# Kernel optimization log

Measured on AMD Instinct MI355X. Metric: run time of the kernel, lower is better.

Reference implementation:

```python
import jax, jax.numpy as jnp
import numpy as np
from jax import lax

B, L, DM = 2, 1024, 1024
DIN, DSTATE, DCONV, DTRANK = 2048, 16, 4, 64


def setup_inputs() -> dict:
    key = jax.random.key(0)
    ks = jax.random.split(key, 8)
    s = 0.02
    x = jax.random.normal(ks[0], (B, L, DM), jnp.float32)
    in_proj_w = jax.random.normal(ks[1], (2 * DIN, DM), jnp.float32) * s
    conv_w = jax.random.normal(ks[2], (DIN, 1, DCONV), jnp.float32) * 0.2
    conv_b = jnp.zeros((DIN,), jnp.float32)
    x_proj_w = jax.random.normal(ks[3], (DTRANK + 2 * DSTATE, DIN), jnp.float32) * s
    dt_proj_w = jax.random.normal(ks[4], (DIN, DTRANK), jnp.float32) * s
    dt_proj_b = jnp.full((DIN,), -4.0, jnp.float32)  # small init dt after softplus
    # S4D-real init: A_log = log(1..d_state) per channel
    A_log = jnp.log(jnp.broadcast_to(jnp.arange(1, DSTATE + 1, dtype=jnp.float32), (DIN, DSTATE)))
    D_skip = jnp.ones((DIN,), jnp.float32)
    out_proj_w = jax.random.normal(ks[5], (DM, DIN), jnp.float32) * s
    return {
        "x": x, "norm_w": jnp.ones((DM,), jnp.float32), "norm_b": jnp.zeros((DM,), jnp.float32),
        "in_proj_w": in_proj_w, "conv_w": conv_w, "conv_b": conv_b,
        "x_proj_w": x_proj_w, "dt_proj_w": dt_proj_w, "dt_proj_b": dt_proj_b,
        "A_log": A_log, "D_skip": D_skip, "out_proj_w": out_proj_w,
    }


def _layernorm(x, w, b, eps=1e-5):
    mu = jnp.mean(x, axis=-1, keepdims=True)
    var = jnp.mean(jnp.square(x - mu), axis=-1, keepdims=True)
    return (x - mu) * lax.rsqrt(var + eps) * w + b


def _mamba(h, in_proj_w, conv_w, conv_b, x_proj_w, dt_proj_w, dt_proj_b, A_log, D_skip, out_proj_w):
    # h: [B, L, DM]
    xz = jnp.einsum('bld,ed->ble', h, in_proj_w)          # [B, L, 2*DIN]
    xm, z = jnp.split(xz, 2, axis=-1)                     # each [B, L, DIN]
    # causal depthwise conv1d over time
    xc = jnp.transpose(xm, (0, 2, 1))                     # [B, DIN, L]
    xc = jnp.pad(xc, ((0, 0), (0, 0), (DCONV - 1, 0)))
    xc = lax.conv_general_dilated(xc, conv_w, (1,), 'VALID',
                                  dimension_numbers=('NCH', 'OIH', 'NCH'),
                                  feature_group_count=DIN)
    xc = xc + conv_b[None, :, None]
    xc = jnp.transpose(xc, (0, 2, 1))                     # [B, L, DIN]
    xc = jax.nn.silu(xc)
    # input-dependent SSM parameters
    x_dbl = jnp.einsum('bld,ed->ble', xc, x_proj_w)       # [B, L, DTRANK+2N]
    dt, Bm, Cm = jnp.split(x_dbl, [DTRANK, DTRANK + DSTATE], axis=-1)
    dt = jax.nn.softplus(jnp.einsum('blr,dr->bld', dt, dt_proj_w) + dt_proj_b)  # [B, L, DIN]
    A = -jnp.exp(A_log)                                   # [DIN, N]
    deltaA = jnp.exp(dt[..., None] * A)                   # [B, L, DIN, N]
    deltaBu = dt[..., None] * Bm[:, :, None, :] * xc[..., None]  # [B, L, DIN, N]
    # sequential selective scan over time
    dA_t = jnp.transpose(deltaA, (1, 0, 2, 3))            # [L, B, DIN, N]
    dBu_t = jnp.transpose(deltaBu, (1, 0, 2, 3))
    C_t = jnp.transpose(Cm, (1, 0, 2))                    # [L, B, N]

    def step(hs, inp):
        dA, dBu, Ct = inp
        hs = dA * hs + dBu                                # [B, DIN, N]
        y = jnp.einsum('bdn,bn->bd', hs, Ct)
        return hs, y

    h0 = jnp.zeros((B, DIN, DSTATE), xc.dtype)
    _, ys = lax.scan(step, h0, (dA_t, dBu_t, C_t))        # ys: [L, B, DIN]
    y = jnp.transpose(ys, (1, 0, 2)) + xc * D_skip        # [B, L, DIN]
    y = y * jax.nn.silu(z)
    return jnp.einsum('bld,ed->ble', y, out_proj_w)       # [B, L, DM]


def reference(x, norm_w, norm_b, in_proj_w, conv_w, conv_b, x_proj_w,
              dt_proj_w, dt_proj_b, A_log, D_skip, out_proj_w):
    h = _layernorm(x, norm_w, norm_b)
    return x + _mamba(h, in_proj_w, conv_w, conv_b, x_proj_w,
                      dt_proj_w, dt_proj_b, A_log, D_skip, out_proj_w)
```

## Files before the change

### kernel.cpp

```cpp
#include <hip/hip_runtime.h>


typedef unsigned short u16;
typedef unsigned int u32;

typedef __bf16 bf16x8 __attribute__((ext_vector_type(8)));
typedef float f32x4 __attribute__((ext_vector_type(4)));

#define SCAN_G 8
#define NSTATE 65536

#if __has_builtin(__builtin_amdgcn_exp2f)
#define EXP2F(x) __builtin_amdgcn_exp2f(x)
#else
#define EXP2F(x) exp2f(x)
#endif
#define LOG2E 1.44269504f

__device__ __forceinline__ u16 f2bf(float f) {
  u32 u = __float_as_uint(f);
  u32 r = u + 0x7FFFu + ((u >> 16) & 1u);
  return (u16)(r >> 16);
}
__device__ __forceinline__ float bf2f(u16 v) {
  return __uint_as_float(((u32)v) << 16);
}

__device__ __forceinline__ void lds_load16(const u16* g, u16* l) {
  __builtin_amdgcn_global_load_lds(
      (const __attribute__((address_space(1))) u32*)g,
      (__attribute__((address_space(3))) u32*)l, 16, 0, 0);
}

__global__ __launch_bounds__(256) void convert_all_kernel(
    const float* __restrict__ w0, const float* __restrict__ w1,
    const float* __restrict__ w2, const float* __restrict__ w3,
    u16* __restrict__ o0, u16* __restrict__ o1,
    u16* __restrict__ o2, u16* __restrict__ o3) {
  const int i = blockIdx.x * 256 + threadIdx.x;
  if (i < 4194304) {
    o0[i] = f2bf(w0[i]);
  } else if (i < 4390912) {
    const int j = i - 4194304;
    o1[j] = f2bf(w1[j]);
  } else if (i < 4521984) {
    const int j = i - 4390912;
    o2[j] = f2bf(w2[j]);
  } else if (i < 6619136) {
    const int j = i - 4521984;
    o3[j] = f2bf(w3[j]);
  }
}

__global__ __launch_bounds__(256) void ln_bf16_kernel(
    const float* __restrict__ x, const float* __restrict__ w,
    const float* __restrict__ b, u16* __restrict__ h) {
  const int row = blockIdx.x;
  const int tid = threadIdx.x;
  const float4 v = ((const float4*)(x + (size_t)row * 1024))[tid];
  float s = v.x + v.y + v.z + v.w;
  float s2 = v.x * v.x + v.y * v.y + v.z * v.z + v.w * v.w;
  for (int off = 32; off >= 1; off >>= 1) {
    s += __shfl_xor(s, off);
    s2 += __shfl_xor(s2, off);
  }
  __shared__ float red[8];
  const int wave = tid >> 6;
  if ((tid & 63) == 0) { red[wave * 2] = s; red[wave * 2 + 1] = s2; }
  __syncthreads();
  s = red[0] + red[2] + red[4] + red[6];
  s2 = red[1] + red[3] + red[5] + red[7];
  const float mu = s * (1.0f / 1024.0f);
  const float var = s2 * (1.0f / 1024.0f) - mu * mu;
  const float rstd = rsqrtf(var + 1e-5f);
  const float4 wv = ((const float4*)w)[tid];
  const float4 bv = ((const float4*)b)[tid];
  ushort4 o;
  o.x = f2bf((v.x - mu) * rstd * wv.x + bv.x);
  o.y = f2bf((v.y - mu) * rstd * wv.y + bv.y);
  o.z = f2bf((v.z - mu) * rstd * wv.z + bv.z);
  o.w = f2bf((v.w - mu) * rstd * wv.w + bv.w);
  ((ushort4*)(h + (size_t)row * 1024))[tid] = o;
}

template <int EPI, int SPLITK>
__global__ __launch_bounds__(256) void gemm_bt(
    const u16* __restrict__ A, const u16* __restrict__ W,
    void* __restrict__ C, const float* __restrict__ extra,
    int M, int N, int K) {
  const int n0 = blockIdx.x * 64;
  const int m0 = blockIdx.y * 64;
  const int ks = (SPLITK > 1) ? blockIdx.z : 0;
  const int kLen = K / SPLITK;
  const int kOff = ks * kLen;
  __shared__ u16 As[64 * 32];
  __shared__ u16 Ws[64 * 32];
  const int tid = threadIdx.x;
  const int wave = tid >> 6;
  const int lane = tid & 63;
  const int wm = (wave >> 1) * 32;
  const int wn = (wave & 1) * 32;
  const int lrow = tid >> 2;
  const int lcg = (tid & 3) * 8;
  const int arow = m0 + lrow;
  const int wrow = n0 + lrow;
  f32x4 acc[2][2];
#pragma unroll
  for (int i = 0; i < 2; ++i)
#pragma unroll
    for (int j = 0; j < 2; ++j) acc[i][j] = (f32x4){0.f, 0.f, 0.f, 0.f};

  const int fm = lane & 15;
  const int fk = (lane >> 4) * 8;

  for (int k0 = kOff; k0 < kOff + kLen; k0 += 32) {
    uint4 av = *(const uint4*)(A + (size_t)arow * K + k0 + lcg);
    uint4 wv = make_uint4(0u, 0u, 0u, 0u);
    if (wrow < N) wv = *(const uint4*)(W + (size_t)wrow * K + k0 + lcg);
    __syncthreads();
    *(uint4*)(As + lrow * 32 + lcg) = av;
    *(uint4*)(Ws + lrow * 32 + lcg) = wv;
    __syncthreads();
    bf16x8 a0 = *(const bf16x8*)(As + (wm + fm) * 32 + fk);
    bf16x8 a1 = *(const bf16x8*)(As + (wm + 16 + fm) * 32 + fk);
    bf16x8 b0 = *(const bf16x8*)(Ws + (wn + fm) * 32 + fk);
    bf16x8 b1 = *(const bf16x8*)(Ws + (wn + 16 + fm) * 32 + fk);
    acc[0][0] = __builtin_amdgcn_mfma_f32_16x16x32_bf16(a0, b0, acc[0][0], 0, 0, 0);
    acc[0][1] = __builtin_amdgcn_mfma_f32_16x16x32_bf16(a0, b1, acc[0][1], 0, 0, 0);
    acc[1][0] = __builtin_amdgcn_mfma_f32_16x16x32_bf16(a1, b0, acc[1][0], 0, 0, 0);
    acc[1][1] = __builtin_amdgcn_mfma_f32_16x16x32_bf16(a1, b1, acc[1][1], 0, 0, 0);
  }

  const int col = lane & 15;
  const int rbase = (lane >> 4) * 4;
#pragma unroll
  for (int tm = 0; tm < 2; ++tm)
#pragma unroll
    for (int tn = 0; tn < 2; ++tn)
#pragma unroll
      for (int r = 0; r < 4; ++r) {
        int m = m0 + wm + tm * 16 + rbase + r;
        int n = n0 + wn + tn * 16 + col;
        if (n < N) {
          float v = acc[tm][tn][r];
          if (EPI == 0) {
            ((float*)C)[(size_t)ks * M * N + (size_t)m * N + n] = v;
          } else {
            v += extra[n];
            v = (v > 20.f) ? v : log1pf(__expf(v));
            ((u16*)C)[(size_t)m * N + n] = f2bf(v);
          }
        }
      }
}

template <int EPI, int SPLITK>
__global__ __launch_bounds__(256) void gemm128_kernel(
    const u16* __restrict__ A, const u16* __restrict__ W,
    u16* __restrict__ Cout, int M, int N, int K) {
  const int n0 = blockIdx.x * 128;
  const int m0 = blockIdx.y * 128;
  const int ks = (SPLITK > 1) ? blockIdx.z : 0;
  const int kLen = K / SPLITK;
  const int k0 = ks * kLen;
  __shared__ u16 As[128 * 32];
  __shared__ u16 Ws[128 * 32];
  const int tid = threadIdx.x;
  const int wave = tid >> 6;
  const int lane = tid & 63;
  const int wm = (wave >> 1) * 64;
  const int wn = (wave & 1) * 64;
  f32x4 acc[4][4];
#pragma unroll
  for (int i = 0; i < 4; ++i)
#pragma unroll
    for (int j = 0; j < 4; ++j) acc[i][j] = (f32x4){0.f, 0.f, 0.f, 0.f};

  const int fm = lane & 15;
  const int fk = (lane >> 4) * 8;
  const int sr = lane >> 2;
  const int sc = (lane & 3) * 8;
  const u16* gA = A + (size_t)(m0 + wave * 32 + sr) * K + k0 + sc;
  const u16* gB = W + (size_t)(n0 + wave * 32 + sr) * K + k0 + sc;
  u16* lA = As + wave * 1024;
  u16* lB = Ws + wave * 1024;

  for (int kk = 0; kk < kLen; kk += 32) {
    __syncthreads();
    lds_load16(gA + kk, lA);
    lds_load16(gA + (size_t)16 * K + kk, lA + 512);
    lds_load16(gB + kk, lB);
    lds_load16(gB + (size_t)16 * K + kk, lB + 512);
    __syncthreads();
    bf16x8 af[4], bfr[4];
#pragma unroll
    for (int i = 0; i < 4; ++i)
      af[i] = *(const bf16x8*)(As + (wm + i * 16 + fm) * 32 + fk);
#pragma unroll
    for (int j = 0; j < 4; ++j)
      bfr[j] = *(const bf16x8*)(Ws + (wn + j * 16 + fm) * 32 + fk);
#pragma unroll
    for (int i = 0; i < 4; ++i)
#pragma unroll
      for (int j = 0; j < 4; ++j)
        acc[i][j] = __builtin_amdgcn_mfma_f32_16x16x32_bf16(af[i], bfr[j], acc[i][j], 0, 0, 0);
  }

  const int col = lane & 15;
  const int rb = (lane >> 4) * 4;
#pragma unroll
  for (int i = 0; i < 4; ++i)
#pragma unroll
    for (int j = 0; j < 4; ++j)
#pragma unroll
      for (int r = 0; r < 4; ++r) {
        const int m = m0 + wm + i * 16 + rb + r;
        const int n = n0 + wn + j * 16 + col;
        if (EPI == 4)
          Cout[(size_t)m * N + n] = f2bf(acc[i][j][r]);
        else
          Cout[(size_t)ks * M * N + (size_t)m * N + n] = f2bf(acc[i][j][r]);
      }
}

__global__ __launch_bounds__(256) void xproj_comb_kernel(
    const float* __restrict__ part, float* __restrict__ xdbl,
    u16* __restrict__ dtr) {
  const int i = blockIdx.x * 256 + threadIdx.x;
  const float v = part[i] + part[i + 196608] + part[i + 2 * 196608] +
                  part[i + 3 * 196608];
  xdbl[i] = v;
  const int m = i / 96;
  const int c = i - m * 96;
  if (c < 64) dtr[(size_t)m * 64 + c] = f2bf(v);
}

__global__ __launch_bounds__(256) void out_comb_kernel(
    const u16* __restrict__ part, const float* __restrict__ x,
    float* __restrict__ out) {
  const int i4 = (blockIdx.x * 256 + threadIdx.x) * 4;
  const float4 xv = *(const float4*)&x[i4];
  float a0 = xv.x, a1 = xv.y, a2 = xv.z, a3 = xv.w;
#pragma unroll
  for (int ks = 0; ks < 4; ++ks) {
    ushort4 pv = *(const ushort4*)&part[(size_t)ks * 2097152 + i4];
    a0 += bf2f(pv.x); a1 += bf2f(pv.y); a2 += bf2f(pv.z); a3 += bf2f(pv.w);
  }
  float4 o = {a0, a1, a2, a3};
  *(float4*)&out[i4] = o;
}

__global__ __launch_bounds__(256) void conv_silu_kernel(
    const u16* __restrict__ xzb, const float* __restrict__ cw,
    const float* __restrict__ cb, u16* __restrict__ xcb) {
  const int idx = blockIdx.x * 256 + threadIdx.x;
  const int d = idx & 2047;
  const int m = idx >> 11;
  const int l = m & 1023;
  const float4 wv = ((const float4*)cw)[d];
  const float w4[4] = {wv.x, wv.y, wv.z, wv.w};
  float acc = cb[d];
#pragma unroll
  for (int k = 0; k < 4; ++k) {
    int lk = l + k - 3;
    if (lk >= 0) acc += bf2f(xzb[(size_t)(m + k - 3) * 4096 + d]) * w4[k];
  }
  const float sv = acc / (1.0f + __expf(-acc));
  xcb[idx] = f2bf(sv);
}

template <int CTRL>
__device__ __forceinline__ float dpp_add(float x) {
  int yi = __builtin_amdgcn_update_dpp(0, __float_as_int(x), CTRL, 0xF, 0xF, true);
  return x + __int_as_float(yi);
}

__global__ __launch_bounds__(256) void scan_pass1_kernel(
    const u16* __restrict__ dtb, const u16* __restrict__ xcb,
    const float* __restrict__ xdbl, const float* __restrict__ A_log,
    float* __restrict__ hend, float* __restrict__ prodA) {
  const int bx = blockIdx.x;
  const int g = bx & 7;
  const int d0 = ((bx >> 3) & 127) * 16;
  const int b = bx >> 10;
  const int tid = threadIdx.x;
  const int dg = tid >> 4;
  const int n = tid & 15;
  const int d = d0 + dg;
  const float a2 = -__expf(A_log[(size_t)d * 16 + n]) * LOG2E;
  float h = 0.f, cs = 0.f;

  __shared__ float sdd[64][16][2];
  __shared__ float sB[64][16];

  const int ss = tid >> 2, q = tid & 3;

  for (int c = 0; c < 2; ++c) {
    const int mb = b * 1024 + g * 128 + c * 64;
    {
      const ushort4 d4 = *(const ushort4*)&dtb[(size_t)(mb + ss) * 2048 + d0 + q * 4];
      const ushort4 x4 = *(const ushort4*)&xcb[(size_t)(mb + ss) * 2048 + d0 + q * 4];
      const float t0 = bf2f(d4.x), t1 = bf2f(d4.y), t2 = bf2f(d4.z), t3 = bf2f(d4.w);
      float4 p0 = {t0, t0 * bf2f(x4.x), t1, t1 * bf2f(x4.y)};
      float4 p1 = {t2, t2 * bf2f(x4.z), t3, t3 * bf2f(x4.w)};
      *(float4*)&sdd[ss][q * 4][0] = p0;
      *(float4*)&sdd[ss][q * 4 + 2][0] = p1;
      *(float4*)&sB[ss][q * 4] =
          *(const float4*)&xdbl[(size_t)(mb + ss) * 96 + 64 + q * 4];
    }
    __syncthreads();
#pragma unroll 8
    for (int s = 0; s < 64; ++s) {
      const float2 ddv = *(const float2*)&sdd[s][dg][0];
      const float Bn = sB[s][n];
      const float da = EXP2F(ddv.x * a2);
      h = __builtin_fmaf(da, h, ddv.y * Bn);
      cs += ddv.x;
    }
    __syncthreads();
  }
  const int sid = ((b * 2048 + d) << 4) + n;
  hend[g * NSTATE + sid] = h;
  prodA[g * NSTATE + sid] = EXP2F(a2 * cs);
}

__global__ __launch_bounds__(256) void scan_pass2_kernel(
    const u16* __restrict__ dtb, const u16* __restrict__ xcb,
    const u16* __restrict__ xzb, const float* __restrict__ xdbl,
    const float* __restrict__ A_log, const float* __restrict__ Dsk,
    const float* __restrict__ hend, const float* __restrict__ prodA,
    u16* __restrict__ yb) {
  const int bx = blockIdx.x;
  const int g = bx & 7;
  const int d0 = ((bx >> 3) & 127) * 16;
  const int b = bx >> 10;
  const int tid = threadIdx.x;
  const int dg = tid >> 4;
  const int n = tid & 15;
  const int d = d0 + dg;
  const float a2 = -__expf(A_log[(size_t)d * 16 + n]) * LOG2E;
  const int sid = ((b * 2048 + d) << 4) + n;
  float h = 0.f;
  for (int gp = 0; gp < g; ++gp)
    h = prodA[gp * NSTATE + sid] * h + hend[gp * NSTATE + sid];
  const int dw = d0 + (tid & 15);
  const float Dw = Dsk[dw];

  __shared__ float sdd[64][16][2];
  __shared__ float sbc[64][16][2];
  __shared__ float sy[64][16];

  const int ss = tid >> 2, q = tid & 3;

  for (int c = 0; c < 2; ++c) {
    const int mb = b * 1024 + g * 128 + c * 64;
    {
      const ushort4 d4 = *(const ushort4*)&dtb[(size_t)(mb + ss) * 2048 + d0 + q * 4];
      const ushort4 x4 = *(const ushort4*)&xcb[(size_t)(mb + ss) * 2048 + d0 + q * 4];
      const float t0 = bf2f(d4.x), t1 = bf2f(d4.y), t2 = bf2f(d4.z), t3 = bf2f(d4.w);
      float4 p0 = {t0, t0 * bf2f(x4.x), t1, t1 * bf2f(x4.y)};
      float4 p1 = {t2, t2 * bf2f(x4.z), t3, t3 * bf2f(x4.w)};
      *(float4*)&sdd[ss][q * 4][0] = p0;
      *(float4*)&sdd[ss][q * 4 + 2][0] = p1;
      const float4 b4 = *(const float4*)&xdbl[(size_t)(mb + ss) * 96 + 64 + q * 4];
      const float4 c4 = *(const float4*)&xdbl[(size_t)(mb + ss) * 96 + 80 + q * 4];
      sbc[ss][q * 4 + 0][0] = b4.x; sbc[ss][q * 4 + 1][0] = b4.y;
      sbc[ss][q * 4 + 2][0] = b4.z; sbc[ss][q * 4 + 3][0] = b4.w;
      sbc[ss][q * 4 + 0][1] = c4.x; sbc[ss][q * 4 + 1][1] = c4.y;
      sbc[ss][q * 4 + 2][1] = c4.z; sbc[ss][q * 4 + 3][1] = c4.w;
    }
    __syncthreads();
#pragma unroll 8
    for (int s = 0; s < 64; ++s) {
      const float2 ddv = *(const float2*)&sdd[s][dg][0];
      const float2 bcv = *(const float2*)&sbc[s][n][0];
      const float da = EXP2F(ddv.x * a2);
      h = __builtin_fmaf(da, h, ddv.y * bcv.x);
      float p = h * bcv.y;
      p = dpp_add<0x111>(p);
      p = dpp_add<0x112>(p);
      p = dpp_add<0x114>(p);
      p = dpp_add<0x118>(p);
      if (n == 15) sy[s][dg] = p;
    }
    __syncthreads();
#pragma unroll
    for (int k = 0; k < 4; ++k) {
      const int idx = k * 256 + tid;
      const int s = idx >> 4;
      const int row = mb + s;
      const float zv = bf2f(xzb[(size_t)row * 4096 + 2048 + dw]);
      const float xcv = bf2f(xcb[(size_t)row * 2048 + dw]);
      const float sz = zv / (1.0f + __expf(-zv));
      const float yv = (sy[s][tid & 15] + xcv * Dw) * sz;
      yb[(size_t)row * 2048 + dw] = f2bf(yv);
    }
    __syncthreads();
  }
}

extern "C" void kernel_launch(void* const* d_in, const int* in_sizes, int n_in,
                              void* d_out, int out_size, void* d_ws, size_t ws_size,
                              hipStream_t stream) {
  const float* x        = (const float*)d_in[0];
  const float* norm_w   = (const float*)d_in[1];
  const float* norm_b   = (const float*)d_in[2];
  const float* in_projw = (const float*)d_in[3];
  const float* conv_w   = (const float*)d_in[4];
  const float* conv_b   = (const float*)d_in[5];
  const float* x_projw  = (const float*)d_in[6];
  const float* dt_projw = (const float*)d_in[7];
  const float* dt_projb = (const float*)d_in[8];
  const float* A_log    = (const float*)d_in[9];
  const float* D_skip   = (const float*)d_in[10];
  const float* out_projw= (const float*)d_in[11];
  float* out = (float*)d_out;

  char* p = (char*)d_ws;
  auto alloc = [&](size_t bytes) {
    char* r = p;
    p += (bytes + 255) & ~(size_t)255;
    return r;
  };
  u16* xzb    = (u16*)alloc(2048ULL * 4096 * 2);
  u16* xcb    = (u16*)alloc(2048ULL * 2048 * 2);
  u16* dtb16  = (u16*)alloc(2048ULL * 2048 * 2);
  float* xdbl = (float*)alloc(2048ULL * 96 * 4);
  u16* h_bf   = (u16*)alloc(2048ULL * 1024 * 2);
  u16* ybf    = (u16*)alloc(2048ULL * 2048 * 2);
  u16* dtr    = (u16*)alloc(2048ULL * 64 * 2);
  u16* Wi     = (u16*)alloc(4096ULL * 1024 * 2);
  u16* Wx     = (u16*)alloc(96ULL * 2048 * 2);
  u16* Wdt    = (u16*)alloc(2048ULL * 64 * 2);
  u16* Wo     = (u16*)alloc(1024ULL * 2048 * 2);
  float* hend = (float*)alloc((size_t)SCAN_G * NSTATE * 4);
  float* prodA= (float*)alloc((size_t)SCAN_G * NSTATE * 4);
  float* xpart= (float*)alloc(4ULL * 2048 * 96 * 4);
  u16* opart  = xzb;
  (void)ws_size; (void)in_sizes; (void)n_in; (void)out_size;

  convert_all_kernel<<<25856, 256, 0, stream>>>(in_projw, x_projw, dt_projw,
                                                out_projw, Wi, Wx, Wdt, Wo);

  ln_bf16_kernel<<<2048, 256, 0, stream>>>(x, norm_w, norm_b, h_bf);

  gemm128_kernel<4, 1><<<dim3(32, 16), 256, 0, stream>>>(h_bf, Wi, xzb, 2048, 4096, 1024);

  conv_silu_kernel<<<16384, 256, 0, stream>>>(xzb, conv_w, conv_b, xcb);

  gemm_bt<0, 4><<<dim3(2, 32, 4), 256, 0, stream>>>(xcb, Wx, xpart, nullptr, 2048, 96, 2048);
  xproj_comb_kernel<<<768, 256, 0, stream>>>(xpart, xdbl, dtr);

  gemm_bt<2, 1><<<dim3(32, 32), 256, 0, stream>>>(dtr, Wdt, dtb16, dt_projb, 2048, 2048, 64);

  scan_pass1_kernel<<<2048, 256, 0, stream>>>(dtb16, xcb, xdbl, A_log, hend, prodA);
  scan_pass2_kernel<<<2048, 256, 0, stream>>>(dtb16, xcb, xzb, xdbl, A_log, D_skip,
                                              hend, prodA, ybf);

  gemm128_kernel<3, 4><<<dim3(8, 16, 4), 256, 0, stream>>>(ybf, Wo, opart, 2048, 1024, 2048);
  out_comb_kernel<<<2048, 256, 0, stream>>>(opart, x, out);
}
```

Baseline: 249.5 us.

## Restructure selective scan to one channel per thread with 16 register states

The scan kernels now assign one channel per thread, holding all 16 states in registers. The C reduction becomes a per-thread FMA chain instead of a DPP cross-lane sum. The time axis is split into 32 chunks of 32 steps, and a new combine kernel computes every chunk's initial state once, so pass2 no longer replays the carried states redundantly per block. B/C rows are read directly from global (broadcast across the block), and dt/xc are packed into one shared word. The costs are fewer blocks (512), a third launch, an extra hinit buffer, and per-step global loads of B/C.

```diff
diff --git a/kernel.cpp b/kernel.cpp
--- a/kernel.cpp
+++ b/kernel.cpp
@@ -7,7 +7,8 @@
 typedef __bf16 bf16x8 __attribute__((ext_vector_type(8)));
 typedef float f32x4 __attribute__((ext_vector_type(4)));
 
-#define SCAN_G 8
+#define SCAN_G 32
+#define SCAN_T 32
 #define NSTATE 65536
 
 #if __has_builtin(__builtin_amdgcn_exp2f)
@@ -269,133 +270,175 @@
   xcb[idx] = f2bf(sv);
 }
 
-template <int CTRL>
-__device__ __forceinline__ float dpp_add(float x) {
-  int yi = __builtin_amdgcn_update_dpp(0, __float_as_int(x), CTRL, 0xF, 0xF, true);
-  return x + __int_as_float(yi);
-}
 
 __global__ __launch_bounds__(256) void scan_pass1_kernel(
     const u16* __restrict__ dtb, const u16* __restrict__ xcb,
     const float* __restrict__ xdbl, const float* __restrict__ A_log,
     float* __restrict__ hend, float* __restrict__ prodA) {
   const int bx = blockIdx.x;
-  const int g = bx & 7;
-  const int d0 = ((bx >> 3) & 127) * 16;
-  const int b = bx >> 10;
+  const int d0 = (bx & 7) * 256;
+  const int b = (bx >> 3) & 1;
+  const int g = bx >> 4;
   const int tid = threadIdx.x;
-  const int dg = tid >> 4;
-  const int n = tid & 15;
-  const int d = d0 + dg;
-  const float a2 = -__expf(A_log[(size_t)d * 16 + n]) * LOG2E;
-  float h = 0.f, cs = 0.f;
-
-  __shared__ float sdd[64][16][2];
-  __shared__ float sB[64][16];
-
-  const int ss = tid >> 2, q = tid & 3;
-
-  for (int c = 0; c < 2; ++c) {
-    const int mb = b * 1024 + g * 128 + c * 64;
-    {
-      const ushort4 d4 = *(const ushort4*)&dtb[(size_t)(mb + ss) * 2048 + d0 + q * 4];
-      const ushort4 x4 = *(const ushort4*)&xcb[(size_t)(mb + ss) * 2048 + d0 + q * 4];
-      const float t0 = bf2f(d4.x), t1 = bf2f(d4.y), t2 = bf2f(d4.z), t3 = bf2f(d4.w);
-      float4 p0 = {t0, t0 * bf2f(x4.x), t1, t1 * bf2f(x4.y)};
-      float4 p1 = {t2, t2 * bf2f(x4.z), t3, t3 * bf2f(x4.w)};
-      *(float4*)&sdd[ss][q * 4][0] = p0;
-      *(float4*)&sdd[ss][q * 4 + 2][0] = p1;
-      *(float4*)&sB[ss][q * 4] =
-          *(const float4*)&xdbl[(size_t)(mb + ss) * 96 + 64 + q * 4];
+  const int d = d0 + tid;
+  const int mb = b * 1024 + g * SCAN_T;
+
+  float a2[16];
+#pragma unroll
+  for (int q = 0; q < 4; ++q) {
+    float4 al = *(const float4*)&A_log[(size_t)d * 16 + q * 4];
+    a2[q * 4 + 0] = -__expf(al.x) * LOG2E;
+    a2[q * 4 + 1] = -__expf(al.y) * LOG2E;
+    a2[q * 4 + 2] = -__expf(al.z) * LOG2E;
+    a2[q * 4 + 3] = -__expf(al.w) * LOG2E;
+  }
+
+  __shared__ u32 sdx[SCAN_T][256];
+
+#pragma unroll
+  for (int i = tid * 4; i < SCAN_T * 256; i += 1024) {
+    const int s = i >> 8, dl = i & 255;
+    ushort4 d4 = *(const ushort4*)&dtb[(size_t)(mb + s) * 2048 + d0 + dl];
+    ushort4 x4 = *(const ushort4*)&xcb[(size_t)(mb + s) * 2048 + d0 + dl];
+    uint4 pk;
+    pk.x = (u32)d4.x | ((u32)x4.x << 16);
+    pk.y = (u32)d4.y | ((u32)x4.y << 16);
+    pk.z = (u32)d4.z | ((u32)x4.z << 16);
+    pk.w = (u32)d4.w | ((u32)x4.w << 16);
+    *(uint4*)&sdx[s][dl] = pk;
+  }
+  __syncthreads();
+
+  float h[16];
+#pragma unroll
+  for (int n = 0; n < 16; ++n) h[n] = 0.f;
+  float cs = 0.f;
+
+  for (int s = 0; s < SCAN_T; ++s) {
+    const u32 u = sdx[s][tid];
+    const float dtv = __uint_as_float(u << 16);
+    const float xcv = __uint_as_float(u & 0xFFFF0000u);
+    const float du = dtv * xcv;
+    const float* Brow = xdbl + (size_t)(mb + s) * 96 + 64;
+    const float4 B0 = *(const float4*)(Brow + 0);
+    const float4 B1 = *(const float4*)(Brow + 4);
+    const float4 B2 = *(const float4*)(Brow + 8);
+    const float4 B3 = *(const float4*)(Brow + 12);
+    const float Bv[16] = {B0.x, B0.y, B0.z, B0.w, B1.x, B1.y, B1.z, B1.w,
+                          B2.x, B2.y, B2.z, B2.w, B3.x, B3.y, B3.z, B3.w};
+#pragma unroll
+    for (int n = 0; n < 16; ++n) {
+      const float da = EXP2F(dtv * a2[n]);
+      h[n] = __builtin_fmaf(da, h[n], du * Bv[n]);
     }
-    __syncthreads();
+    cs += dtv;
+  }
+
+  const size_t base = ((size_t)(g * 2 + b) * 2048 + d) * 16;
+#pragma unroll
+  for (int q = 0; q < 4; ++q) {
+    float4 hv = {h[q * 4], h[q * 4 + 1], h[q * 4 + 2], h[q * 4 + 3]};
+    *(float4*)&hend[base + q * 4] = hv;
+    float4 pv = {EXP2F(a2[q * 4] * cs), EXP2F(a2[q * 4 + 1] * cs),
+                 EXP2F(a2[q * 4 + 2] * cs), EXP2F(a2[q * 4 + 3] * cs)};
+    *(float4*)&prodA[base + q * 4] = pv;
+  }
+}
+
+__global__ __launch_bounds__(256) void scan_combine_kernel(
+    const float* __restrict__ hend, const float* __restrict__ prodA,
+    float* __restrict__ hinit) {
+  const int sid = blockIdx.x * 256 + threadIdx.x;
+  float H = 0.f;
 #pragma unroll 8
-    for (int s = 0; s < 64; ++s) {
-      const float2 ddv = *(const float2*)&sdd[s][dg][0];
-      const float Bn = sB[s][n];
-      const float da = EXP2F(ddv.x * a2);
-      h = __builtin_fmaf(da, h, ddv.y * Bn);
-      cs += ddv.x;
-    }
-    __syncthreads();
-  }
-  const int sid = ((b * 2048 + d) << 4) + n;
-  hend[g * NSTATE + sid] = h;
-  prodA[g * NSTATE + sid] = EXP2F(a2 * cs);
+  for (int g = 0; g < SCAN_G; ++g) {
+    hinit[g * NSTATE + sid] = H;
+    H = prodA[g * NSTATE + sid] * H + hend[g * NSTATE + sid];
+  }
 }
 
 __global__ __launch_bounds__(256) void scan_pass2_kernel(
     const u16* __restrict__ dtb, const u16* __restrict__ xcb,
     const u16* __restrict__ xzb, const float* __restrict__ xdbl,
     const float* __restrict__ A_log, const float* __restrict__ Dsk,
-    const float* __restrict__ hend, const float* __restrict__ prodA,
-    u16* __restrict__ yb) {
+    const float* __restrict__ hinit, u16* __restrict__ yb) {
   const int bx = blockIdx.x;
-  const int g = bx & 7;
-  const int d0 = ((bx >> 3) & 127) * 16;
-  const int b = bx >> 10;
+  const int d0 = (bx & 7) * 256;
+  const int b = (bx >> 3) & 1;
+  const int g = bx >> 4;
   const int tid = threadIdx.x;
-  const int dg = tid >> 4;
-  const int n = tid & 15;
-  const int d = d0 + dg;
-  const float a2 = -__expf(A_log[(size_t)d * 16 + n]) * LOG2E;
-  const int sid = ((b * 2048 + d) << 4) + n;
-  float h = 0.f;
-  for (int gp = 0; gp < g; ++gp)
-    h = prodA[gp * NSTATE + sid] * h + hend[gp * NSTATE + sid];
-  const int dw = d0 + (tid & 15);
-  const float Dw = Dsk[dw];
-
-  __shared__ float sdd[64][16][2];
-  __shared__ float sbc[64][16][2];
-  __shared__ float sy[64][16];
-
-  const int ss = tid >> 2, q = tid & 3;
-
-  for (int c = 0; c < 2; ++c) {
-    const int mb = b * 1024 + g * 128 + c * 64;
-    {
-      const ushort4 d4 = *(const ushort4*)&dtb[(size_t)(mb + ss) * 2048 + d0 + q * 4];
-      const ushort4 x4 = *(const ushort4*)&xcb[(size_t)(mb + ss) * 2048 + d0 + q * 4];
-      const float t0 = bf2f(d4.x), t1 = bf2f(d4.y), t2 = bf2f(d4.z), t3 = bf2f(d4.w);
-      float4 p0 = {t0, t0 * bf2f(x4.x), t1, t1 * bf2f(x4.y)};
-      float4 p1 = {t2, t2 * bf2f(x4.z), t3, t3 * bf2f(x4.w)};
-      *(float4*)&sdd[ss][q * 4][0] = p0;
-      *(float4*)&sdd[ss][q * 4 + 2][0] = p1;
-      const float4 b4 = *(const float4*)&xdbl[(size_t)(mb + ss) * 96 + 64 + q * 4];
-      const float4 c4 = *(const float4*)&xdbl[(size_t)(mb + ss) * 96 + 80 + q * 4];
-      sbc[ss][q * 4 + 0][0] = b4.x; sbc[ss][q * 4 + 1][0] = b4.y;
-      sbc[ss][q * 4 + 2][0] = b4.z; sbc[ss][q * 4 + 3][0] = b4.w;
-      sbc[ss][q * 4 + 0][1] = c4.x; sbc[ss][q * 4 + 1][1] = c4.y;
-      sbc[ss][q * 4 + 2][1] = c4.z; sbc[ss][q * 4 + 3][1] = c4.w;
+  const int d = d0 + tid;
+  const int mb = b * 1024 + g * SCAN_T;
+
+  float a2[16];
+#pragma unroll
+  for (int q = 0; q < 4; ++q) {
+    float4 al = *(const float4*)&A_log[(size_t)d * 16 + q * 4];
+    a2[q * 4 + 0] = -__expf(al.x) * LOG2E;
+    a2[q * 4 + 1] = -__expf(al.y) * LOG2E;
+    a2[q * 4 + 2] = -__expf(al.z) * LOG2E;
+    a2[q * 4 + 3] = -__expf(al.w) * LOG2E;
+  }
+  const float Dd = Dsk[d];
+
+  __shared__ u32 sdx[SCAN_T][256];
+  __shared__ u16 sz[SCAN_T][256];
+
+#pragma unroll
+  for (int i = tid * 4; i < SCAN_T * 256; i += 1024) {
+    const int s = i >> 8, dl = i & 255;
+    ushort4 d4 = *(const ushort4*)&dtb[(size_t)(mb + s) * 2048 + d0 + dl];
+    ushort4 x4 = *(const ushort4*)&xcb[(size_t)(mb + s) * 2048 + d0 + dl];
+    uint4 pk;
+    pk.x = (u32)d4.x | ((u32)x4.x << 16);
+    pk.y = (u32)d4.y | ((u32)x4.y << 16);
+    pk.z = (u32)d4.z | ((u32)x4.z << 16);
+    pk.w = (u32)d4.w | ((u32)x4.w << 16);
+    *(uint4*)&sdx[s][dl] = pk;
+    *(ushort4*)&sz[s][dl] =
+        *(const ushort4*)&xzb[(size_t)(mb + s) * 4096 + 2048 + d0 + dl];
+  }
+  __syncthreads();
+
+  float h[16];
+  {
+    const float* hi = hinit + ((size_t)(g * 2 + b) * 2048 + d) * 16;
+#pragma unroll
+    for (int q = 0; q < 4; ++q) {
+      float4 hv = *(const float4*)(hi + q * 4);
+      h[q * 4] = hv.x; h[q * 4 + 1] = hv.y; h[q * 4 + 2] = hv.z; h[q * 4 + 3] = hv.w;
     }
-    __syncthreads();
-#pragma unroll 8
-    for (int s = 0; s < 64; ++s) {
-      const float2 ddv = *(const float2*)&sdd[s][dg][0];
-      const float2 bcv = *(const float2*)&sbc[s][n][0];
-      const float da = EXP2F(ddv.x * a2);
-      h = __builtin_fmaf(da, h, ddv.y * bcv.x);
-      float p = h * bcv.y;
-      p = dpp_add<0x111>(p);
-      p = dpp_add<0x112>(p);
-      p = dpp_add<0x114>(p);
-      p = dpp_add<0x118>(p);
-      if (n == 15) sy[s][dg] = p;
+  }
+
+  for (int s = 0; s < SCAN_T; ++s) {
+    const u32 u = sdx[s][tid];
+    const float dtv = __uint_as_float(u << 16);
+    const float xcv = __uint_as_float(u & 0xFFFF0000u);
+    const float du = dtv * xcv;
+    const float* Xrow = xdbl + (size_t)(mb + s) * 96 + 64;
+    const float4 B0 = *(const float4*)(Xrow + 0);
+    const float4 B1 = *(const float4*)(Xrow + 4);
+    const float4 B2 = *(const float4*)(Xrow + 8);
+    const float4 B3 = *(const float4*)(Xrow + 12);
+    const float4 C0 = *(const float4*)(Xrow + 16);
+    const float4 C1 = *(const float4*)(Xrow + 20);
+    const float4 C2 = *(const float4*)(Xrow + 24);
+    const float4 C3 = *(const float4*)(Xrow + 28);
+    const float Bv[16] = {B0.x, B0.y, B0.z, B0.w, B1.x, B1.y, B1.z, B1.w,
+                          B2.x, B2.y, B2.z, B2.w, B3.x, B3.y, B3.z, B3.w};
+    const float Cv[16] = {C0.x, C0.y, C0.z, C0.w, C1.x, C1.y, C1.z, C1.w,
+                          C2.x, C2.y, C2.z, C2.w, C3.x, C3.y, C3.z, C3.w};
+    float y = 0.f;
+#pragma unroll
+    for (int n = 0; n < 16; ++n) {
+      const float da = EXP2F(dtv * a2[n]);
+      h[n] = __builtin_fmaf(da, h[n], du * Bv[n]);
+      y = __builtin_fmaf(h[n], Cv[n], y);
     }
-    __syncthreads();
-#pragma unroll
-    for (int k = 0; k < 4; ++k) {
-      const int idx = k * 256 + tid;
-      const int s = idx >> 4;
-      const int row = mb + s;
-      const float zv = bf2f(xzb[(size_t)row * 4096 + 2048 + dw]);
-      const float xcv = bf2f(xcb[(size_t)row * 2048 + dw]);
-      const float sz = zv / (1.0f + __expf(-zv));
-      const float yv = (sy[s][tid & 15] + xcv * Dw) * sz;
-      yb[(size_t)row * 2048 + dw] = f2bf(yv);
-    }
-    __syncthreads();
+    const float zv = bf2f(sz[s][tid]);
+    const float sig = 1.0f / (1.0f + EXP2F(-zv * LOG2E));
+    const float yv = (y + xcv * Dd) * (zv * sig);
+    yb[(size_t)(mb + s) * 2048 + d] = f2bf(yv);
   }
 }
 
@@ -435,6 +478,7 @@
   u16* Wo     = (u16*)alloc(1024ULL * 2048 * 2);
   float* hend = (float*)alloc((size_t)SCAN_G * NSTATE * 4);
   float* prodA= (float*)alloc((size_t)SCAN_G * NSTATE * 4);
+  float* hinit= (float*)alloc((size_t)SCAN_G * NSTATE * 4);
   float* xpart= (float*)alloc(4ULL * 2048 * 96 * 4);
   u16* opart  = xzb;
   (void)ws_size; (void)in_sizes; (void)n_in; (void)out_size;
@@ -453,9 +497,10 @@
 
   gemm_bt<2, 1><<<dim3(32, 32), 256, 0, stream>>>(dtr, Wdt, dtb16, dt_projb, 2048, 2048, 64);
 
-  scan_pass1_kernel<<<2048, 256, 0, stream>>>(dtb16, xcb, xdbl, A_log, hend, prodA);
-  scan_pass2_kernel<<<2048, 256, 0, stream>>>(dtb16, xcb, xzb, xdbl, A_log, D_skip,
-                                              hend, prodA, ybf);
+  scan_pass1_kernel<<<512, 256, 0, stream>>>(dtb16, xcb, xdbl, A_log, hend, prodA);
+  scan_combine_kernel<<<256, 256, 0, stream>>>(hend, prodA, hinit);
+  scan_pass2_kernel<<<512, 256, 0, stream>>>(dtb16, xcb, xzb, xdbl, A_log, D_skip,
+                                             hinit, ybf);
 
   gemm128_kernel<3, 4><<<dim3(8, 16, 4), 256, 0, stream>>>(ybf, Wo, opart, 2048, 1024, 2048);
   out_comb_kernel<<<2048, 256, 0, stream>>>(opart, x, out);
```

Measured after the change: 253.9 us. Within noise of the previous version (+1.8%).
